# Kernel tuning notes

Measured on AMD Instinct MI355X. Metric: run time of the kernel, lower is better.

## Reference

```python
import jax, jax.numpy as jnp
import numpy as np

C = 64
INTER = C // 2  # 32
B, L = 4, 4096


def setup_inputs() -> dict:
    key = jax.random.key(0)
    ks = jax.random.split(key, 9)
    s_in = 1.0 / np.sqrt(C)
    s_inter = 1.0 / np.sqrt(INTER)
    return {
        "x": jax.random.normal(ks[0], (B, C, L), dtype=jnp.float32),
        "g_w": jax.random.normal(ks[1], (INTER, C), dtype=jnp.float32) * s_in,
        "g_b": jax.random.normal(ks[2], (INTER,), dtype=jnp.float32) * s_in,
        "theta_w": jax.random.normal(ks[3], (INTER, C), dtype=jnp.float32) * s_in,
        "theta_b": jax.random.normal(ks[4], (INTER,), dtype=jnp.float32) * s_in,
        "phi_w": jax.random.normal(ks[5], (INTER, C), dtype=jnp.float32) * s_in,
        "phi_b": jax.random.normal(ks[6], (INTER,), dtype=jnp.float32) * s_in,
        # NOTE: original inits W to zero (residual starts as identity); we use small
        # random values so the reference exercises the full computation.
        "W_w": jax.random.normal(ks[7], (C, INTER), dtype=jnp.float32) * s_inter,
        "W_b": jax.random.normal(ks[8], (C,), dtype=jnp.float32) * s_inter,
    }


def reference(x, g_w, g_b, theta_w, theta_b, phi_w, phi_b, W_w, W_b):
    # 1x1 Conv1d == channel matmul: [O,C] x [B,C,L] -> [B,O,L]
    g_x = jnp.einsum('oc,bcl->bol', g_w, x) + g_b[None, :, None]
    theta_x = jnp.einsum('oc,bcl->bol', theta_w, x) + theta_b[None, :, None]
    phi_x = jnp.einsum('oc,bcl->bol', phi_w, x) + phi_b[None, :, None]
    # f[b,l,m] = theta[:,l] . phi[:,m]  (unscaled attention scores, [B,L,L])
    f = jnp.einsum('bol,bom->blm', theta_x, phi_x)
    f_div_C = jax.nn.softmax(f, axis=-1)
    # y[b,o,l] = sum_m f[b,l,m] * g[b,o,m]
    y = jnp.einsum('blm,bom->bol', f_div_C, g_x)
    W_y = jnp.einsum('co,bol->bcl', W_w, y) + W_b[None, :, None]
    return W_y + x
```

## Files before the change

### kernel.cpp

```cpp
#include <hip/hip_runtime.h>

#define Bn 4
#define Cdim 64
#define INTER 32
#define Ln 4096
#define LOG2E 1.44269504088896340736f

typedef _Float16 half_t;
typedef __attribute__((ext_vector_type(8))) _Float16 half8v;
typedef __attribute__((ext_vector_type(4))) short short4v;
typedef __attribute__((ext_vector_type(8))) short short8v;
typedef __attribute__((ext_vector_type(4))) float f32x4;

__device__ __forceinline__ unsigned short f2bf(float f) {
    unsigned u = __float_as_uint(f);
    u += 0x7fffu + ((u >> 16) & 1u);
    return (unsigned short)(u >> 16);
}
__device__ __forceinline__ float bf2f(unsigned short b) {
    return __uint_as_float(((unsigned)b) << 16);
}
__device__ __forceinline__ unsigned pack_bf(float a, float b) {
    unsigned ua = __float_as_uint(a) + 0x8000u;
    unsigned ub = __float_as_uint(b) + 0x8000u;
    return __builtin_amdgcn_perm(ub, ua, 0x07060302);
}
__device__ __forceinline__ void gll16(const void* g, void* l) {
    __builtin_amdgcn_global_load_lds(
        (const __attribute__((address_space(1))) unsigned int*)g,
        (__attribute__((address_space(3))) unsigned int*)l, 16, 0, 0);
}

__global__ void setup_kernel(const float* __restrict__ g_w, const float* __restrict__ g_b,
                             const float* __restrict__ th_w, const float* __restrict__ th_b,
                             const float* __restrict__ ph_w, const float* __restrict__ ph_b,
                             const float* __restrict__ W_w, const float* __restrict__ W_b,
                             half_t* __restrict__ Wcat, float* __restrict__ biasbuf,
                             float* __restrict__ bc, half_t* __restrict__ Wm) {
    int blk = blockIdx.x, tid = threadIdx.x;
    if (blk < 96) {
        int row = blk;
        float v;
        if (row < 32) v = th_w[row * 64 + tid] * LOG2E;
        else if (row < 64) v = ph_w[(row - 32) * 64 + tid];
        else v = g_w[(row - 64) * 64 + tid];
        Wcat[row * 64 + tid] = (half_t)v;
    } else if (blk == 96) {
        for (int i = tid; i < 96; i += 64) {
            float v = (i < 32) ? th_b[i] * LOG2E : (i < 64) ? ph_b[i - 32] : g_b[i - 64];
            biasbuf[i] = v;
        }
    } else if (blk == 97) {
        bc[tid] = W_b[tid];
    } else {
        int l15 = tid & 15, jb = (tid >> 4) * 8;
        for (int mf = 0; mf < 4; mf++) {
            int c = mf * 16 + l15;
            half_t tmp[8];
            for (int j = 0; j < 8; j++) tmp[j] = (half_t)W_w[c * 32 + jb + j];
            float4 v;
            __builtin_memcpy(&v, tmp, 16);
            *(float4*)(Wm + (mf * 64 + tid) * 8) = v;
        }
    }
}

__global__ __launch_bounds__(192) void proj_kernel(
        const float* __restrict__ x, const half_t* __restrict__ Wcat,
        const float* __restrict__ biasbuf,
        half_t* __restrict__ thfrag, half_t* __restrict__ phfrag,
        unsigned short* __restrict__ gfrag) {
    __shared__ half_t sx[64][72];
    int tid = threadIdx.x;
    int b = blockIdx.x >> 6;
    int l0 = (blockIdx.x & 63) << 6;

    for (int i = tid; i < 1024; i += 192) {
        int c = i >> 4, lq = (i & 15) << 2;
        float4 v = *(const float4*)&x[(size_t)(b * 64 + c) * Ln + l0 + lq];
        sx[lq + 0][c] = (half_t)v.x;
        sx[lq + 1][c] = (half_t)v.y;
        sx[lq + 2][c] = (half_t)v.z;
        sx[lq + 3][c] = (half_t)v.w;
    }
    __syncthreads();

    int lane = tid & 63, grp = tid >> 6;
    int l15 = lane & 15, quad = lane >> 4;

    half8v wA[2][2];
#pragma unroll
    for (int mf = 0; mf < 2; mf++)
#pragma unroll
        for (int kk = 0; kk < 2; kk++)
            wA[mf][kk] = *(const half8v*)(Wcat + (grp * 32 + mf * 16 + l15) * 64 +
                                          kk * 32 + quad * 8);
    half8v xB[4][2];
#pragma unroll
    for (int nf = 0; nf < 4; nf++)
#pragma unroll
        for (int kk = 0; kk < 2; kk++)
            xB[nf][kk] = *(const half8v*)&sx[nf * 16 + l15][kk * 32 + quad * 8];

    f32x4 acc[2][4];
    const f32x4 z = {0.f, 0.f, 0.f, 0.f};
#pragma unroll
    for (int mf = 0; mf < 2; mf++)
#pragma unroll
        for (int nf = 0; nf < 4; nf++) {
            f32x4 a = __builtin_amdgcn_mfma_f32_16x16x32_f16(wA[mf][0], xB[nf][0], z, 0, 0, 0);
            acc[mf][nf] = __builtin_amdgcn_mfma_f32_16x16x32_f16(wA[mf][1], xB[nf][1], a, 0, 0, 0);
        }
#pragma unroll
    for (int mf = 0; mf < 2; mf++) {
        float4 bv = *(const float4*)&biasbuf[grp * 32 + mf * 16 + quad * 4];
#pragma unroll
        for (int nf = 0; nf < 4; nf++) {
            acc[mf][nf][0] += bv.x; acc[mf][nf][1] += bv.y;
            acc[mf][nf][2] += bv.z; acc[mf][nf][3] += bv.w;
        }
    }

    if (grp < 2) {
        half_t* F = (grp == 0) ? thfrag : phfrag;
#pragma unroll
        for (int mf = 0; mf < 2; mf++)
#pragma unroll
            for (int nf = 0; nf < 4; nf++) {
                half_t h[4];
                h[0] = (half_t)acc[mf][nf][0]; h[1] = (half_t)acc[mf][nf][1];
                h[2] = (half_t)acc[mf][nf][2]; h[3] = (half_t)acc[mf][nf][3];
                uint2 v;
                __builtin_memcpy(&v, h, 8);
                size_t u = (size_t)(b * 256 + (l0 >> 4) + nf) * 64 +
                           l15 + 16 * (mf * 2 + (quad >> 1));
                *(uint2*)(F + u * 8 + (quad & 1) * 4) = v;
            }
    } else {
#pragma unroll
        for (int mf = 0; mf < 2; mf++)
#pragma unroll
            for (int nf = 0; nf < 4; nf++)
#pragma unroll
                for (int r = 0; r < 4; r++) {
                    size_t u = (size_t)(b * 256 + (l0 >> 4) + nf) * 64 +
                               (quad * 4 + r) + 16 * (l15 >> 2);
                    gfrag[u * 8 + mf * 4 + (l15 & 3)] = f2bf(acc[mf][nf][r]);
                }
    }
}

__global__ __launch_bounds__(256, 4) void attn_kernel(
        const half_t* __restrict__ thfrag, const half_t* __restrict__ phfrag,
        const unsigned short* __restrict__ gfrag,
        unsigned short* __restrict__ part, float* __restrict__ Sden,
        int KC, int CH) {
    __shared__ uint4 sbuf[2][512];

    int tid = threadIdx.x, lane = tid & 63, widx = tid >> 6;
    int l15 = lane & 15, quad = lane >> 4;

    int blk = blockIdx.x;
    int b = blk / (32 * KC);
    int rem = blk % (32 * KC);
    int qblk = rem / KC, kc = rem % KC;
    int qbase = qblk * 128 + widx * 32;
    int k0 = kc * CH;

    half8v th[2];
#pragma unroll
    for (int qf = 0; qf < 2; qf++)
        th[qf] = *(const half8v*)(thfrag +
                                  ((size_t)(b * 256 + (qbase >> 4) + qf) * 64 + lane) * 8);

    f32x4 acc[2][2];
#pragma unroll
    for (int qf = 0; qf < 2; qf++) {
        acc[qf][0] = (f32x4){0.f, 0.f, 0.f, 0.f};
        acc[qf][1] = (f32x4){0.f, 0.f, 0.f, 0.f};
    }
    float lsum[2] = {0.f, 0.f};

    const char* phsrc = (const char*)(phfrag + (size_t)b * 256 * 512);
    const char* gsrc  = (const char*)(gfrag + (size_t)b * 256 * 512);
    const f32x4 z = {0.f, 0.f, 0.f, 0.f};

    gll16(phsrc + (size_t)(k0 >> 4) * 1024 + tid * 16, (char*)&sbuf[0][0] + tid * 16);
    gll16(gsrc + (size_t)(k0 >> 4) * 1024 + tid * 16, (char*)&sbuf[0][256] + tid * 16);
    __syncthreads();

    int cb = 0;
    for (int kt = k0; kt < k0 + CH; kt += 64) {
        if (kt + 64 < k0 + CH) {
            gll16(phsrc + (size_t)((kt + 64) >> 4) * 1024 + tid * 16,
                  (char*)&sbuf[cb ^ 1][0] + tid * 16);
            gll16(gsrc + (size_t)((kt + 64) >> 4) * 1024 + tid * 16,
                  (char*)&sbuf[cb ^ 1][256] + tid * 16);
        }
        const half_t* sph = (const half_t*)&sbuf[cb][0];
        const unsigned short* sg = (const unsigned short*)&sbuf[cb][256];
#pragma unroll
        for (int kf = 0; kf < 4; kf++) {
            half8v phA = *(const half8v*)(sph + kf * 512 + lane * 8);
            short8v g8 = *(const short8v*)(sg + kf * 512 + lane * 8);
            short4v ga0 = __builtin_shufflevector(g8, g8, 0, 1, 2, 3);
            short4v ga1 = __builtin_shufflevector(g8, g8, 4, 5, 6, 7);
#pragma unroll
            for (int qf = 0; qf < 2; qf++) {
                f32x4 s = __builtin_amdgcn_mfma_f32_16x16x32_f16(phA, th[qf], z, 0, 0, 0);
                float p0 = __builtin_amdgcn_exp2f(s[0]);
                float p1 = __builtin_amdgcn_exp2f(s[1]);
                float p2 = __builtin_amdgcn_exp2f(s[2]);
                float p3 = __builtin_amdgcn_exp2f(s[3]);
                lsum[qf] += (p0 + p1) + (p2 + p3);
                union { short4v s4; uint2 u2; } pb;
                pb.u2.x = pack_bf(p0, p1);
                pb.u2.y = pack_bf(p2, p3);
                acc[qf][0] = __builtin_amdgcn_mfma_f32_16x16x16bf16_1k(ga0, pb.s4,
                                                                      acc[qf][0], 0, 0, 0);
                acc[qf][1] = __builtin_amdgcn_mfma_f32_16x16x16bf16_1k(ga1, pb.s4,
                                                                      acc[qf][1], 0, 0, 0);
            }
        }
        __syncthreads();
        cb ^= 1;
    }

#pragma unroll
    for (int qf = 0; qf < 2; qf++) {
        float v = lsum[qf];
        v += __shfl_xor(v, 16);
        v += __shfl_xor(v, 32);
        lsum[qf] = v;
    }
    size_t sb = (size_t)(b * KC + kc) * Ln + qbase;
    if (lane < 16) {
        Sden[sb + lane] = lsum[0];
        Sden[sb + 16 + lane] = lsum[1];
    }
    size_t pbase = (size_t)(b * KC + kc) * 32 * Ln;
#pragma unroll
    for (int qf = 0; qf < 2; qf++)
#pragma unroll
        for (int cf = 0; cf < 2; cf++)
#pragma unroll
            for (int r = 0; r < 4; r++) {
                int c = cf * 16 + quad * 4 + r;
                part[pbase + (size_t)c * Ln + qbase + qf * 16 + l15] =
                    f2bf(acc[qf][cf][r]);
            }
}

__global__ __launch_bounds__(256) void merge1_kernel(
        const unsigned short* __restrict__ part, const float* __restrict__ Sden,
        half_t* __restrict__ ybar, int KC) {
    int t = blockIdx.x * 256 + threadIdx.x;
    int l4 = (t & 1023) << 2;
    int j = (t >> 10) & 31;
    int b = t >> 15;
    float num[4] = {0.f, 0.f, 0.f, 0.f};
    float den[4] = {0.f, 0.f, 0.f, 0.f};
    for (int kc = 0; kc < KC; kc++) {
        ushort4 y4 = *(const ushort4*)&part[((size_t)((b * KC + kc) * 32) + j) * Ln + l4];
        float4 lc = *(const float4*)&Sden[(size_t)(b * KC + kc) * Ln + l4];
        num[0] += bf2f(y4.x); num[1] += bf2f(y4.y);
        num[2] += bf2f(y4.z); num[3] += bf2f(y4.w);
        den[0] += lc.x; den[1] += lc.y; den[2] += lc.z; den[3] += lc.w;
    }
#pragma unroll
    for (int i = 0; i < 4; i++) {
        int l = l4 + i;
        size_t u = (size_t)(b * 256 + (l >> 4)) * 64 + (l & 15) + 16 * (j >> 3);
        ybar[u * 8 + (j & 7)] = (half_t)(num[i] / den[i]);
    }
}

__global__ __launch_bounds__(256) void merge2_kernel(
        const half_t* __restrict__ ybar, const half_t* __restrict__ Wm,
        const float* __restrict__ bc, const float* __restrict__ x,
        float* __restrict__ out) {
    int tid = threadIdx.x, lane = tid & 63, widx = tid >> 6;
    int l15 = lane & 15, quad = lane >> 4;
    int b = blockIdx.x >> 6;
    int t16 = (blockIdx.x & 63) * 4 + widx;
    int l = (t16 << 4) + l15;

    half8v yB = *(const half8v*)(ybar + ((size_t)(b * 256 + t16) * 64 + lane) * 8);
    const f32x4 z = {0.f, 0.f, 0.f, 0.f};
    f32x4 acc[4];
#pragma unroll
    for (int mf = 0; mf < 4; mf++) {
        half8v wA = *(const half8v*)(Wm + (mf * 64 + lane) * 8);
        acc[mf] = __builtin_amdgcn_mfma_f32_16x16x32_f16(wA, yB, z, 0, 0, 0);
    }
#pragma unroll
    for (int mf = 0; mf < 4; mf++)
#pragma unroll
        for (int r = 0; r < 4; r++) {
            int c = mf * 16 + quad * 4 + r;
            size_t idx = (size_t)(b * 64 + c) * Ln + l;
            out[idx] = acc[mf][r] + bc[c] + x[idx];
        }
}

extern "C" void kernel_launch(void* const* d_in, const int* in_sizes, int n_in,
                              void* d_out, int out_size, void* d_ws, size_t ws_size,
                              hipStream_t stream) {
    const float* x    = (const float*)d_in[0];
    const float* g_w  = (const float*)d_in[1];
    const float* g_b  = (const float*)d_in[2];
    const float* th_w = (const float*)d_in[3];
    const float* th_b = (const float*)d_in[4];
    const float* ph_w = (const float*)d_in[5];
    const float* ph_b = (const float*)d_in[6];
    const float* W_w  = (const float*)d_in[7];
    const float* W_b  = (const float*)d_in[8];
    float* out = (float*)d_out;

    char* w = (char*)d_ws;
    const size_t off_th   = 0;
    const size_t off_ph   = 1048576;
    const size_t off_g    = 2097152;
    const size_t off_ybar = 3145728;
    const size_t off_Wcat = 4194304;
    const size_t off_bias = 4206592;
    const size_t off_bc   = 4207104;
    const size_t off_Wm   = 4207360;
    const size_t off_Sden = 4211712;

    int KC = 8;
    size_t off_part = 0;
    while (true) {
        off_part = off_Sden + (size_t)KC * (Bn * Ln * 4);
        off_part = (off_part + 255) & ~(size_t)255;
        size_t need = off_part + (size_t)KC * ((size_t)Bn * 32 * Ln * 2);
        if (need <= ws_size || KC == 1) break;
        KC >>= 1;
    }

    half_t* thfrag = (half_t*)(w + off_th);
    half_t* phfrag = (half_t*)(w + off_ph);
    unsigned short* gfrag = (unsigned short*)(w + off_g);
    half_t* ybar   = (half_t*)(w + off_ybar);
    half_t* Wcat   = (half_t*)(w + off_Wcat);
    float* biasbuf = (float*)(w + off_bias);
    float* bc      = (float*)(w + off_bc);
    half_t* Wm     = (half_t*)(w + off_Wm);
    float* Sden    = (float*)(w + off_Sden);
    unsigned short* part = (unsigned short*)(w + off_part);

    int CH = Ln / KC;

    setup_kernel<<<99, 64, 0, stream>>>(g_w, g_b, th_w, th_b, ph_w, ph_b, W_w, W_b,
                                        Wcat, biasbuf, bc, Wm);
    proj_kernel<<<Bn * 64, 192, 0, stream>>>(x, Wcat, biasbuf, thfrag, phfrag, gfrag);
    attn_kernel<<<Bn * 32 * KC, 256, 0, stream>>>(thfrag, phfrag, gfrag, part, Sden,
                                                  KC, CH);
    merge1_kernel<<<512, 256, 0, stream>>>(part, Sden, ybar, KC);
    merge2_kernel<<<Bn * 64, 256, 0, stream>>>(ybar, Wm, bc, x, out);
}
```

Before: 104.6 us.

## Fuse merge kernels, compute softmax denominator via MFMA, stage g writes through LDS

Merges the two merge kernels into one, which reduces the KC partial sums and feeds the normalized y straight into the output projection MFMA, dropping the ybar round trip and one launch. In the attention loop, the per-row exp sum now comes from an extra bf16 MFMA against a ones vector instead of scalar adds plus shuffles. This moves work from VALU to the matrix unit but sums bf16-rounded probabilities. The proj kernel stages g fragments in LDS so global writes become coalesced 16-byte stores. It syncs only with s_waitcnt and no barrier, which is enough only if each wave reads back just its own LDS writes.

```diff
diff --git a/kernel.cpp b/kernel.cpp
--- a/kernel.cpp
+++ b/kernel.cpp
@@ -71,6 +71,7 @@
         half_t* __restrict__ thfrag, half_t* __restrict__ phfrag,
         unsigned short* __restrict__ gfrag) {
     __shared__ half_t sx[64][72];
+    __shared__ unsigned short sg[2048];
     int tid = threadIdx.x;
     int b = blockIdx.x >> 6;
     int l0 = (blockIdx.x & 63) << 6;
@@ -143,10 +144,17 @@
             for (int nf = 0; nf < 4; nf++)
 #pragma unroll
                 for (int r = 0; r < 4; r++) {
-                    size_t u = (size_t)(b * 256 + (l0 >> 4) + nf) * 64 +
-                               (quad * 4 + r) + 16 * (l15 >> 2);
-                    gfrag[u * 8 + mf * 4 + (l15 & 3)] = f2bf(acc[mf][nf][r]);
+                    int lu = nf * 64 + (quad * 4 + r) + 16 * (l15 >> 2);
+                    sg[lu * 8 + mf * 4 + (l15 & 3)] = f2bf(acc[mf][nf][r]);
                 }
+        __builtin_amdgcn_s_waitcnt(0);
+        size_t base = (size_t)(b * 256 + (l0 >> 4)) * 512;
+#pragma unroll
+        for (int s = 0; s < 4; s++) {
+            int i = lane + s * 64;
+            uint4 v = ((const uint4*)sg)[i];
+            *(uint4*)(gfrag + base + (size_t)i * 8) = v;
+        }
     }
 }
 
@@ -173,13 +181,17 @@
         th[qf] = *(const half8v*)(thfrag +
                                   ((size_t)(b * 256 + (qbase >> 4) + qf) * 64 + lane) * 8);
 
-    f32x4 acc[2][2];
+    unsigned short oh = (l15 == 0) ? 0x3F80 : 0;
+    short4v ones;
+    ones[0] = (short)oh; ones[1] = (short)oh; ones[2] = (short)oh; ones[3] = (short)oh;
+
+    f32x4 acc[2][2], accd[2];
 #pragma unroll
     for (int qf = 0; qf < 2; qf++) {
         acc[qf][0] = (f32x4){0.f, 0.f, 0.f, 0.f};
         acc[qf][1] = (f32x4){0.f, 0.f, 0.f, 0.f};
-    }
-    float lsum[2] = {0.f, 0.f};
+        accd[qf]   = (f32x4){0.f, 0.f, 0.f, 0.f};
+    }
 
     const char* phsrc = (const char*)(phfrag + (size_t)b * 256 * 512);
     const char* gsrc  = (const char*)(gfrag + (size_t)b * 256 * 512);
@@ -212,7 +224,6 @@
                 float p1 = __builtin_amdgcn_exp2f(s[1]);
                 float p2 = __builtin_amdgcn_exp2f(s[2]);
                 float p3 = __builtin_amdgcn_exp2f(s[3]);
-                lsum[qf] += (p0 + p1) + (p2 + p3);
                 union { short4v s4; uint2 u2; } pb;
                 pb.u2.x = pack_bf(p0, p1);
                 pb.u2.y = pack_bf(p2, p3);
@@ -220,23 +231,18 @@
                                                                       acc[qf][0], 0, 0, 0);
                 acc[qf][1] = __builtin_amdgcn_mfma_f32_16x16x16bf16_1k(ga1, pb.s4,
                                                                       acc[qf][1], 0, 0, 0);
+                accd[qf] = __builtin_amdgcn_mfma_f32_16x16x16bf16_1k(ones, pb.s4,
+                                                                    accd[qf], 0, 0, 0);
             }
         }
         __syncthreads();
         cb ^= 1;
     }
 
-#pragma unroll
-    for (int qf = 0; qf < 2; qf++) {
-        float v = lsum[qf];
-        v += __shfl_xor(v, 16);
-        v += __shfl_xor(v, 32);
-        lsum[qf] = v;
-    }
     size_t sb = (size_t)(b * KC + kc) * Ln + qbase;
-    if (lane < 16) {
-        Sden[sb + lane] = lsum[0];
-        Sden[sb + 16 + lane] = lsum[1];
+    if (quad == 0) {
+        Sden[sb + l15] = accd[0][0];
+        Sden[sb + 16 + l15] = accd[1][0];
     }
     size_t pbase = (size_t)(b * KC + kc) * 32 * Ln;
 #pragma unroll
@@ -251,41 +257,32 @@
             }
 }
 
-__global__ __launch_bounds__(256) void merge1_kernel(
+__global__ __launch_bounds__(256) void merge_kernel(
         const unsigned short* __restrict__ part, const float* __restrict__ Sden,
-        half_t* __restrict__ ybar, int KC) {
-    int t = blockIdx.x * 256 + threadIdx.x;
-    int l4 = (t & 1023) << 2;
-    int j = (t >> 10) & 31;
-    int b = t >> 15;
-    float num[4] = {0.f, 0.f, 0.f, 0.f};
-    float den[4] = {0.f, 0.f, 0.f, 0.f};
-    for (int kc = 0; kc < KC; kc++) {
-        ushort4 y4 = *(const ushort4*)&part[((size_t)((b * KC + kc) * 32) + j) * Ln + l4];
-        float4 lc = *(const float4*)&Sden[(size_t)(b * KC + kc) * Ln + l4];
-        num[0] += bf2f(y4.x); num[1] += bf2f(y4.y);
-        num[2] += bf2f(y4.z); num[3] += bf2f(y4.w);
-        den[0] += lc.x; den[1] += lc.y; den[2] += lc.z; den[3] += lc.w;
-    }
-#pragma unroll
-    for (int i = 0; i < 4; i++) {
-        int l = l4 + i;
-        size_t u = (size_t)(b * 256 + (l >> 4)) * 64 + (l & 15) + 16 * (j >> 3);
-        ybar[u * 8 + (j & 7)] = (half_t)(num[i] / den[i]);
-    }
-}
-
-__global__ __launch_bounds__(256) void merge2_kernel(
-        const half_t* __restrict__ ybar, const half_t* __restrict__ Wm,
-        const float* __restrict__ bc, const float* __restrict__ x,
-        float* __restrict__ out) {
+        const half_t* __restrict__ Wm, const float* __restrict__ bc,
+        const float* __restrict__ x, float* __restrict__ out, int KC) {
     int tid = threadIdx.x, lane = tid & 63, widx = tid >> 6;
     int l15 = lane & 15, quad = lane >> 4;
     int b = blockIdx.x >> 6;
     int t16 = (blockIdx.x & 63) * 4 + widx;
     int l = (t16 << 4) + l15;
 
-    half8v yB = *(const half8v*)(ybar + ((size_t)(b * 256 + t16) * 64 + lane) * 8);
+    float den = 0.f;
+    for (int kc = 0; kc < KC; kc++) den += Sden[(size_t)(b * KC + kc) * Ln + l];
+    float inv = 1.f / den;
+
+    float num[8] = {0.f, 0.f, 0.f, 0.f, 0.f, 0.f, 0.f, 0.f};
+    for (int kc = 0; kc < KC; kc++) {
+        size_t base = ((size_t)((b * KC + kc) * 32) + quad * 8) * Ln + l;
+#pragma unroll
+        for (int j = 0; j < 8; j++) num[j] += bf2f(part[base + (size_t)j * Ln]);
+    }
+    half_t yh[8];
+#pragma unroll
+    for (int j = 0; j < 8; j++) yh[j] = (half_t)(num[j] * inv);
+    half8v yB;
+    __builtin_memcpy(&yB, yh, 16);
+
     const f32x4 z = {0.f, 0.f, 0.f, 0.f};
     f32x4 acc[4];
 #pragma unroll
@@ -294,13 +291,16 @@
         acc[mf] = __builtin_amdgcn_mfma_f32_16x16x32_f16(wA, yB, z, 0, 0, 0);
     }
 #pragma unroll
-    for (int mf = 0; mf < 4; mf++)
+    for (int mf = 0; mf < 4; mf++) {
+        float4 bv = *(const float4*)&bc[mf * 16 + quad * 4];
 #pragma unroll
         for (int r = 0; r < 4; r++) {
             int c = mf * 16 + quad * 4 + r;
             size_t idx = (size_t)(b * 64 + c) * Ln + l;
-            out[idx] = acc[mf][r] + bc[c] + x[idx];
-        }
+            float bb = (r == 0) ? bv.x : (r == 1) ? bv.y : (r == 2) ? bv.z : bv.w;
+            out[idx] = acc[mf][r] + bb + x[idx];
+        }
+    }
 }
 
 extern "C" void kernel_launch(void* const* d_in, const int* in_sizes, int n_in,
@@ -321,7 +321,6 @@
     const size_t off_th   = 0;
     const size_t off_ph   = 1048576;
     const size_t off_g    = 2097152;
-    const size_t off_ybar = 3145728;
     const size_t off_Wcat = 4194304;
     const size_t off_bias = 4206592;
     const size_t off_bc   = 4207104;
@@ -341,7 +340,6 @@
     half_t* thfrag = (half_t*)(w + off_th);
     half_t* phfrag = (half_t*)(w + off_ph);
     unsigned short* gfrag = (unsigned short*)(w + off_g);
-    half_t* ybar   = (half_t*)(w + off_ybar);
     half_t* Wcat   = (half_t*)(w + off_Wcat);
     float* biasbuf = (float*)(w + off_bias);
     float* bc      = (float*)(w + off_bc);
@@ -356,6 +354,5 @@
     proj_kernel<<<Bn * 64, 192, 0, stream>>>(x, Wcat, biasbuf, thfrag, phfrag, gfrag);
     attn_kernel<<<Bn * 32 * KC, 256, 0, stream>>>(thfrag, phfrag, gfrag, part, Sden,
                                                   KC, CH);
-    merge1_kernel<<<512, 256, 0, stream>>>(part, Sden, ybar, KC);
-    merge2_kernel<<<Bn * 64, 256, 0, stream>>>(ybar, Wm, bc, x, out);
-}
+    merge_kernel<<<Bn * 64, 256, 0, stream>>>(part, Sden, Wm, bc, x, out, KC);
+}
```

Result: no change. 102.9 us (-1.7%).
